# Performance work log

Measured on AMD Instinct MI355X. Metric: run time of the kernel, lower is better.

The kernel has to match this reference:

```python
import jax, jax.numpy as jnp
import numpy as np

N_EMBD = 384
N_HEAD = 6
HEAD_SIZE = N_EMBD // N_HEAD  # 64
B, T, S = 128, 256, 256
EPS = 1e-5


def setup_inputs() -> dict:
    key = jax.random.key(0)
    ks = jax.random.split(key, 20)
    w = lambda k, shape: (jax.random.normal(k, shape, dtype=jnp.float32) * 0.02)
    inp = {
        'x': jax.random.normal(ks[0], (B, T, N_EMBD), dtype=jnp.float32),
        'encoder_output': jax.random.normal(ks[1], (B, S, N_EMBD), dtype=jnp.float32),
        # masked self-attention heads (stacked over heads): [H, C, D]
        'wq1': w(ks[2], (N_HEAD, N_EMBD, HEAD_SIZE)),
        'wk1': w(ks[3], (N_HEAD, N_EMBD, HEAD_SIZE)),
        'wv1': w(ks[4], (N_HEAD, N_EMBD, HEAD_SIZE)),
        'proj1_w': w(ks[5], (N_EMBD, N_EMBD)),
        'proj1_b': jnp.zeros((N_EMBD,), jnp.float32),
        # cross-attention heads
        'wq2': w(ks[6], (N_HEAD, N_EMBD, HEAD_SIZE)),
        'wk2': w(ks[7], (N_HEAD, N_EMBD, HEAD_SIZE)),
        'wv2': w(ks[8], (N_HEAD, N_EMBD, HEAD_SIZE)),
        'proj2_w': w(ks[9], (N_EMBD, N_EMBD)),
        'proj2_b': jnp.zeros((N_EMBD,), jnp.float32),
        # feed-forward
        'ffn_w1': w(ks[10], (N_EMBD, 4 * N_EMBD)),
        'ffn_b1': jnp.zeros((4 * N_EMBD,), jnp.float32),
        'ffn_w2': w(ks[11], (4 * N_EMBD, N_EMBD)),
        'ffn_b2': jnp.zeros((N_EMBD,), jnp.float32),
        # layernorms
        'ln1_g': jnp.ones((N_EMBD,), jnp.float32), 'ln1_b': jnp.zeros((N_EMBD,), jnp.float32),
        'ln2_g': jnp.ones((N_EMBD,), jnp.float32), 'ln2_b': jnp.zeros((N_EMBD,), jnp.float32),
        'ln3_g': jnp.ones((N_EMBD,), jnp.float32), 'ln3_b': jnp.zeros((N_EMBD,), jnp.float32),
    }
    return inp


def _layernorm(x, g, b):
    mu = jnp.mean(x, axis=-1, keepdims=True)
    var = jnp.mean(jnp.square(x - mu), axis=-1, keepdims=True)
    return (x - mu) * jax.lax.rsqrt(var + EPS) * g + b


def _mha(xq, xkv, wq, wk, wv, proj_w, proj_b, causal):
    # NOTE: source scales by C**-0.5 with C = n_embd (not head_size)
    scale = jnp.asarray(N_EMBD, xq.dtype) ** -0.5
    q = jnp.einsum('btc,hcd->bhtd', xq, wq)
    k = jnp.einsum('bsc,hcd->bhsd', xkv, wk)
    v = jnp.einsum('bsc,hcd->bhsd', xkv, wv)
    wei = jnp.einsum('bhtd,bhsd->bhts', q, k) * scale
    if causal:
        Tq, Tk = xq.shape[1], xkv.shape[1]
        mask = jnp.tril(jnp.ones((Tq, Tk), dtype=bool))
        wei = jnp.where(mask, wei, jnp.asarray(-jnp.inf, wei.dtype))
    p = jax.nn.softmax(wei, axis=-1)  # dropout omitted (eval mode)
    o = jnp.einsum('bhts,bhsd->bhtd', p, v)
    Bq, H, Tq, D = o.shape
    o = o.transpose(0, 2, 1, 3).reshape(Bq, Tq, H * D)  # concat heads
    return o @ proj_w + proj_b


def reference(x, encoder_output,
              wq1, wk1, wv1, proj1_w, proj1_b,
              wq2, wk2, wv2, proj2_w, proj2_b,
              ffn_w1, ffn_b1, ffn_w2, ffn_b2,
              ln1_g, ln1_b, ln2_g, ln2_b, ln3_g, ln3_b):
    # x = x + masked self-attn(ln1(x))
    x = x + _mha(_layernorm(x, ln1_g, ln1_b), _layernorm(x, ln1_g, ln1_b),
                 wq1, wk1, wv1, proj1_w, proj1_b, causal=True)
    # x = x + cross-attn(ln2(x), encoder_output)  (no mask)
    x = x + _mha(_layernorm(x, ln2_g, ln2_b), encoder_output,
                 wq2, wk2, wv2, proj2_w, proj2_b, causal=False)
    # x = x + ffwd(ln3(x))
    h = _layernorm(x, ln3_g, ln3_b)
    x = x + (jax.nn.relu(h @ ffn_w1 + ffn_b1) @ ffn_w2 + ffn_b2)
    return x
```

## Files before the change

### kernel.cpp

```cpp
#include <hip/hip_runtime.h>
#include <hip/hip_bf16.h>

#define BB 128
#define TT 256
#define CC 384
#define HH 6
#define DD 64
#define NTOK 32768

typedef __attribute__((ext_vector_type(8))) short short8;
typedef __attribute__((ext_vector_type(4))) float f32x4;

__device__ __forceinline__ unsigned short f2bf(float f) {
  union { float f; unsigned int u; } v; v.f = f;
  unsigned int r = v.u + 0x7fff + ((v.u >> 16) & 1);
  return (unsigned short)(r >> 16);
}

__device__ __forceinline__ void glds16(const void* g, void* l) {
  __builtin_amdgcn_global_load_lds((const __attribute__((address_space(1))) void*)g,
                                   (__attribute__((address_space(3))) void*)l, 16, 0, 0);
}

__device__ __forceinline__ void vm_drain() {
  asm volatile("s_waitcnt vmcnt(0)" ::: "memory");
  __builtin_amdgcn_sched_barrier(0);
}

__global__ __launch_bounds__(256) void pack_all_k(
    const float* __restrict__ wq1, const float* __restrict__ wk1, const float* __restrict__ wv1,
    const float* __restrict__ wq2, const float* __restrict__ wk2, const float* __restrict__ wv2,
    const float* __restrict__ proj1_w, const float* __restrict__ proj2_w,
    const float* __restrict__ ffn_w1, const float* __restrict__ ffn_w2,
    unsigned short* __restrict__ W) {
  int idx = blockIdx.x * 256 + threadIdx.x;
  if (idx < 589824) {
    int sub = idx / 147456, r = idx - sub * 147456;
    const float* src = sub == 0 ? wq1 : sub == 1 ? wk1 : sub == 2 ? wv1 : wq2;
    unsigned short* dst = W + sub * 147456;
    int h = r / 24576, rem = r - h * 24576;
    int c = rem >> 6, d = rem & 63;
    dst[(h * 64 + d) * 384 + c] = f2bf(src[r]);
  } else if (idx < 884736) {
    int t = idx - 589824;
    int sub = t / 147456, r = t - sub * 147456;
    const float* src = sub ? wv2 : wk2;
    unsigned short* dst = W + 589824 + sub * 147456;
    int h = r / 24576, rem = r - h * 24576;
    int c = rem >> 6, d = rem & 63;
    dst[(h * 64 + d) * 384 + c] = f2bf(src[r]);
  } else if (idx < 1179648) {
    int t = idx - 884736;
    int sub = t / 147456, r = t - sub * 147456;
    const float* src = sub ? proj2_w : proj1_w;
    unsigned short* dst = W + 884736 + sub * 147456;
    int c = r / 384, n = r - c * 384;
    dst[n * 384 + c] = f2bf(src[r]);
  } else if (idx < 1769472) {
    int r = idx - 1179648;
    int c = r / 1536, n = r - c * 1536;
    (W + 1179648)[n * 384 + c] = f2bf(ffn_w1[r]);
  } else {
    int r = idx - 1769472;
    int c = r / 384, n = r - c * 384;
    (W + 1769472)[n * 1536 + c] = f2bf(ffn_w2[r]);
  }
}

__global__ __launch_bounds__(256) void ln_k(const float* __restrict__ x,
                                            unsigned short* __restrict__ out,
                                            const float* __restrict__ gamma,
                                            const float* __restrict__ beta) {
  int row = blockIdx.x * 4 + (threadIdx.x >> 6);
  int lane = threadIdx.x & 63;
  const float* xr = x + (size_t)row * CC;
  float v[6];
  float s = 0.f;
#pragma unroll
  for (int j = 0; j < 6; ++j) { v[j] = xr[j * 64 + lane]; s += v[j]; }
#pragma unroll
  for (int m = 1; m < 64; m <<= 1) s += __shfl_xor(s, m);
  float mu = s * (1.0f / CC);
  float vs = 0.f;
#pragma unroll
  for (int j = 0; j < 6; ++j) { float d = v[j] - mu; vs += d * d; }
#pragma unroll
  for (int m = 1; m < 64; m <<= 1) vs += __shfl_xor(vs, m);
  float rs = rsqrtf(vs * (1.0f / CC) + 1e-5f);
  unsigned short* orow = out + (size_t)row * CC;
#pragma unroll
  for (int j = 0; j < 6; ++j) {
    int cidx = j * 64 + lane;
    orow[cidx] = f2bf((v[j] - mu) * rs * gamma[cidx] + beta[cidx]);
  }
}

template <int EPI, bool AF32>
__global__ __launch_bounds__(256) void gemm_k(const void* __restrict__ Ap, int lda,
                                              const unsigned short* __restrict__ Bt, int ldb,
                                              void* __restrict__ Cp, int ldc,
                                              const float* __restrict__ bias,
                                              const float* __restrict__ res, int ldres,
                                              int K, int nx) {
  __shared__ unsigned short smem[16384];
  unsigned short* sA = smem;
  unsigned short* sB = smem + 8192;
  const int tid = threadIdx.x;
  const int chunkg = gridDim.x >> 3;
  const int wg = blockIdx.x;
  const int lg = (wg & 7) * chunkg + (wg >> 3);
  const int bx = lg % nx, by = lg / nx;
  const int m0 = by * 128;
  const int n0 = bx * 128;
  const int wid = tid >> 6, lane = tid & 63;
  const int wr = wid >> 1, wc = wid & 1;
  const int g = lane >> 4, c = lane & 15;

  f32x4 acc[4][4] = {};
  float biasr[4];
  if (EPI >= 1) {
#pragma unroll
    for (int ni = 0; ni < 4; ++ni) biasr[ni] = bias[n0 + wc * 64 + ni * 16 + c];
  }

  for (int k0 = 0; k0 < K; k0 += 64) {
    if constexpr (!AF32) {
#pragma unroll
      for (int t = 0; t < 4; ++t) {
        int chunk = t * 256 + tid;
        int row = chunk >> 3, grp = chunk & 7;
        const unsigned short* Ab = (const unsigned short*)Ap;
        glds16(&Ab[(size_t)(m0 + row) * lda + k0 + ((grp ^ (row & 7)) << 3)], &sA[chunk * 8]);
      }
    } else {
#pragma unroll
      for (int t = 0; t < 4; ++t) {
        int chunk = t * 256 + tid;
        int row = chunk >> 3, grp = chunk & 7;
        int dst = row * 64 + ((grp ^ (row & 7)) << 3);
        const float* Af = (const float*)Ap + (size_t)(m0 + row) * lda + k0 + grp * 8;
        float4 f0 = *(const float4*)Af;
        float4 f1 = *(const float4*)(Af + 4);
        union { unsigned short h[8]; uint4 u; } t2;
        t2.h[0] = f2bf(f0.x); t2.h[1] = f2bf(f0.y); t2.h[2] = f2bf(f0.z); t2.h[3] = f2bf(f0.w);
        t2.h[4] = f2bf(f1.x); t2.h[5] = f2bf(f1.y); t2.h[6] = f2bf(f1.z); t2.h[7] = f2bf(f1.w);
        *(uint4*)&sA[dst] = t2.u;
      }
    }
#pragma unroll
    for (int t = 0; t < 4; ++t) {
      int chunk = t * 256 + tid;
      int row = chunk >> 3, grp = chunk & 7;
      glds16(&Bt[(size_t)(n0 + row) * ldb + k0 + ((grp ^ (row & 7)) << 3)], &sB[chunk * 8]);
    }
    vm_drain();
    __syncthreads();
#pragma unroll
    for (int kk = 0; kk < 2; ++kk) {
      short8 a[4], b[4];
#pragma unroll
      for (int mi = 0; mi < 4; ++mi) {
        int r = wr * 64 + mi * 16 + c;
        a[mi] = *(const short8*)&sA[r * 64 + (((kk * 4 + g) ^ (r & 7)) << 3)];
      }
#pragma unroll
      for (int ni = 0; ni < 4; ++ni) {
        int rb = wc * 64 + ni * 16 + c;
        b[ni] = *(const short8*)&sB[rb * 64 + (((kk * 4 + g) ^ (rb & 7)) << 3)];
      }
#pragma unroll
      for (int mi = 0; mi < 4; ++mi)
#pragma unroll
        for (int ni = 0; ni < 4; ++ni)
          acc[mi][ni] = __builtin_amdgcn_mfma_f32_16x16x32_bf16(a[mi], b[ni], acc[mi][ni], 0, 0, 0);
    }
    __syncthreads();
  }

  if (EPI <= 1) {
#pragma unroll
    for (int mi = 0; mi < 4; ++mi)
#pragma unroll
      for (int ni = 0; ni < 4; ++ni)
#pragma unroll
        for (int i = 0; i < 4; ++i) {
          int row = wr * 64 + mi * 16 + g * 4 + i;
          int col = wc * 64 + ni * 16 + c;
          float v = acc[mi][ni][i];
          if (EPI == 1) v = fmaxf(v + biasr[ni], 0.f);
          int gsw = (col >> 3) ^ ((row >> 2) & 7);
          smem[row * 128 + gsw * 8 + (col & 7)] = f2bf(v);
        }
    __syncthreads();
#pragma unroll
    for (int it = 0; it < 8; ++it) {
      int chunk = it * 256 + tid;
      int row = chunk >> 4, c16 = chunk & 15;
      int gsw = c16 ^ ((row >> 2) & 7);
      *(uint4*)&((unsigned short*)Cp)[(size_t)(m0 + row) * ldc + n0 + c16 * 8] =
          *(const uint4*)&smem[row * 128 + gsw * 8];
    }
  } else {
#pragma unroll
    for (int mi = 0; mi < 4; ++mi)
#pragma unroll
      for (int ni = 0; ni < 4; ++ni)
#pragma unroll
        for (int i = 0; i < 4; ++i) {
          int row = m0 + wr * 64 + mi * 16 + g * 4 + i;
          int col = n0 + wc * 64 + ni * 16 + c;
          float v = acc[mi][ni][i] + biasr[ni] + res[(size_t)row * ldres + col];
          ((float*)Cp)[(size_t)row * ldc + col] = v;
        }
  }
}

__device__ __forceinline__ int vt_off(int d, int sgrp) {
  return d * 256 + ((((sgrp + (d >> 3)) & 31) ^ (d & 7)) << 3);
}

template <bool CAUSAL>
__global__ __launch_bounds__(512, 2) void attn_k(const unsigned short* __restrict__ QKV,
                                                 unsigned short* __restrict__ O) {
  __shared__ unsigned short Ks[256 * 64];
  __shared__ unsigned short Vt[64 * 256];
  __shared__ unsigned short Ps[8][16 * 40];
  const int bh = blockIdx.x >> 1;
  const int half = blockIdx.x & 1;
  const int b = bh / HH, hh = bh - b * HH;
  const int tid = threadIdx.x, wid = tid >> 6, lane = tid & 63;
  const int g = lane >> 4, c = lane & 15;
  const unsigned short* base = QKV + (size_t)b * TT * 1152;

#pragma unroll
  for (int t = 0; t < 4; ++t) {
    int chunk = t * 512 + tid;
    int s = chunk >> 3, grp = chunk & 7;
    *(uint4*)&Ks[s * 64 + ((grp ^ (s & 7)) << 3)] =
        *(const uint4*)&base[(size_t)s * 1152 + 384 + hh * 64 + grp * 8];
    union { unsigned short h[8]; uint4 u; } tv;
    tv.u = *(const uint4*)&base[(size_t)s * 1152 + 768 + hh * 64 + grp * 8];
#pragma unroll
    for (int j = 0; j < 8; ++j) Vt[vt_off(grp * 8 + j, s >> 3) + (s & 7)] = tv.h[j];
  }
  __syncthreads();

  const float scale = 0.05103103630798287f;
  unsigned short* Pw = &Ps[wid][0];
  const int qr0 = half * 128 + wid * 16;

  short8 aq[2];
#pragma unroll
  for (int kk = 0; kk < 2; ++kk)
    aq[kk] = *(const short8*)&QKV[(size_t)(b * TT + qr0 + c) * 1152 + hh * 64 + kk * 32 + g * 8];

  f32x4 sacc[16] = {};
#pragma unroll
  for (int sj = 0; sj < 16; ++sj) {
    if (!CAUSAL || sj * 16 <= qr0) {
      int rk = sj * 16 + c;
      f32x4 z = sacc[sj];
      z = __builtin_amdgcn_mfma_f32_16x16x32_bf16(
          aq[0], *(const short8*)&Ks[rk * 64 + ((g ^ (rk & 7)) << 3)], z, 0, 0, 0);
      z = __builtin_amdgcn_mfma_f32_16x16x32_bf16(
          aq[1], *(const short8*)&Ks[rk * 64 + (((4 + g) ^ (rk & 7)) << 3)], z, 0, 0, 0);
      sacc[sj] = z;
    }
  }

  float inv[4];
#pragma unroll
  for (int i = 0; i < 4; ++i) {
    const int qr = qr0 + g * 4 + i;
    float mx = -1e30f;
#pragma unroll
    for (int sj = 0; sj < 16; ++sj) {
      if (!CAUSAL || sj * 16 <= qr0) {
        int s = sj * 16 + c;
        float v = sacc[sj][i] * scale;
        if (CAUSAL && s > qr) v = -1e30f;
        sacc[sj][i] = v;
        mx = fmaxf(mx, v);
      }
    }
#pragma unroll
    for (int m = 1; m < 16; m <<= 1) mx = fmaxf(mx, __shfl_xor(mx, m));
    float sum = 0.f;
#pragma unroll
    for (int sj = 0; sj < 16; ++sj) {
      if (!CAUSAL || sj * 16 <= qr0) {
        float p = __expf(sacc[sj][i] - mx);
        sacc[sj][i] = p;
        sum += p;
      }
    }
#pragma unroll
    for (int m = 1; m < 16; m <<= 1) sum += __shfl_xor(sum, m);
    inv[i] = 1.0f / sum;
  }

  f32x4 oacc[4] = {};
#pragma unroll
  for (int sk = 0; sk < 8; ++sk) {
    if (!CAUSAL || sk * 32 <= qr0) {
#pragma unroll
      for (int half_sj = 0; half_sj < 2; ++half_sj) {
        int sj = sk * 2 + half_sj;
#pragma unroll
        for (int i = 0; i < 4; ++i)
          Pw[(g * 4 + i) * 40 + half_sj * 16 + c] = f2bf(sacc[sj][i]);
      }
      short8 ap = *(const short8*)&Pw[c * 40 + g * 8];
#pragma unroll
      for (int dj = 0; dj < 4; ++dj) {
        short8 bv = *(const short8*)&Vt[vt_off(dj * 16 + c, sk * 4 + g)];
        oacc[dj] = __builtin_amdgcn_mfma_f32_16x16x32_bf16(ap, bv, oacc[dj], 0, 0, 0);
      }
    }
  }

  __syncthreads();
#pragma unroll
  for (int dj = 0; dj < 4; ++dj)
#pragma unroll
    for (int i = 0; i < 4; ++i) {
      int lr = wid * 16 + g * 4 + i;
      int col = dj * 16 + c;
      int gsw = (col >> 3) ^ ((lr >> 2) & 7);
      Ks[lr * 64 + gsw * 8 + (col & 7)] = f2bf(oacc[dj][i] * inv[i]);
    }
  __syncthreads();
#pragma unroll
  for (int it = 0; it < 2; ++it) {
    int chunk = it * 512 + tid;
    int row = chunk >> 3, c8 = chunk & 7;
    int gsw = c8 ^ ((row >> 2) & 7);
    *(uint4*)&O[(size_t)(b * TT + half * 128 + row) * CC + hh * 64 + c8 * 8] =
        *(const uint4*)&Ks[row * 64 + gsw * 8];
  }
}

extern "C" void kernel_launch(void* const* d_in, const int* in_sizes, int n_in,
                              void* d_out, int out_size, void* d_ws, size_t ws_size,
                              hipStream_t stream) {
  const float* x = (const float*)d_in[0];
  const float* enc = (const float*)d_in[1];
  const float* wq1 = (const float*)d_in[2];
  const float* wk1 = (const float*)d_in[3];
  const float* wv1 = (const float*)d_in[4];
  const float* proj1_w = (const float*)d_in[5];
  const float* proj1_b = (const float*)d_in[6];
  const float* wq2 = (const float*)d_in[7];
  const float* wk2 = (const float*)d_in[8];
  const float* wv2 = (const float*)d_in[9];
  const float* proj2_w = (const float*)d_in[10];
  const float* proj2_b = (const float*)d_in[11];
  const float* ffn_w1 = (const float*)d_in[12];
  const float* ffn_b1 = (const float*)d_in[13];
  const float* ffn_w2 = (const float*)d_in[14];
  const float* ffn_b2 = (const float*)d_in[15];
  const float* ln1_g = (const float*)d_in[16];
  const float* ln1_b = (const float*)d_in[17];
  const float* ln2_g = (const float*)d_in[18];
  const float* ln2_b = (const float*)d_in[19];
  const float* ln3_g = (const float*)d_in[20];
  const float* ln3_b = (const float*)d_in[21];
  float* out = (float*)d_out;

  char* ws = (char*)d_ws;
  const size_t OFF_A = 0;
  const size_t OFF_X = 50331648;
  const size_t OFF_Q = 75497472;
  const size_t OFF_O = 150994944;
  const size_t OFF_W = 176160768;

  float* xc = (float*)(ws + OFF_A);
  unsigned short* xn = (unsigned short*)(ws + OFF_X);
  unsigned short* qkv = (unsigned short*)(ws + OFF_Q);
  unsigned short* h1 = (unsigned short*)(ws + OFF_Q);
  unsigned short* obuf = (unsigned short*)(ws + OFF_O);
  unsigned short* W = (unsigned short*)(ws + OFF_W);

  unsigned short* Wqkv1t = W + 0;
  unsigned short* Wq2t = W + 442368;
  unsigned short* Wkv2t = W + 589824;
  unsigned short* proj1t = W + 884736;
  unsigned short* proj2t = W + 1032192;
  unsigned short* W1t = W + 1179648;
  unsigned short* W2t = W + 1769472;

  pack_all_k<<<9216, 256, 0, stream>>>(wq1, wk1, wv1, wq2, wk2, wv2,
                                       proj1_w, proj2_w, ffn_w1, ffn_w2, W);

  dim3 blk(256);
  ln_k<<<8192, blk, 0, stream>>>(x, xn, ln1_g, ln1_b);
  gemm_k<0, false><<<2304, blk, 0, stream>>>(xn, 384, Wqkv1t, 384, qkv, 1152,
                                             nullptr, nullptr, 0, 384, 9);
  attn_k<true><<<1536, 512, 0, stream>>>(qkv, obuf);
  gemm_k<2, false><<<768, blk, 0, stream>>>(obuf, 384, proj1t, 384, xc, 384,
                                            proj1_b, x, 384, 384, 3);
  ln_k<<<8192, blk, 0, stream>>>(xc, xn, ln2_g, ln2_b);
  gemm_k<0, false><<<768, blk, 0, stream>>>(xn, 384, Wq2t, 384, qkv, 1152,
                                            nullptr, nullptr, 0, 384, 3);
  gemm_k<0, true><<<1536, blk, 0, stream>>>(enc, 384, Wkv2t, 384, qkv + 384, 1152,
                                            nullptr, nullptr, 0, 384, 6);
  attn_k<false><<<1536, 512, 0, stream>>>(qkv, obuf);
  gemm_k<2, false><<<768, blk, 0, stream>>>(obuf, 384, proj2t, 384, xc, 384,
                                            proj2_b, xc, 384, 384, 3);
  ln_k<<<8192, blk, 0, stream>>>(xc, xn, ln3_g, ln3_b);
  gemm_k<1, false><<<3072, blk, 0, stream>>>(xn, 384, W1t, 384, h1, 1536,
                                             ffn_b1, nullptr, 0, 384, 12);
  gemm_k<2, false><<<768, blk, 0, stream>>>(h1, 1536, W2t, 1536, out, 384,
                                            ffn_b2, xc, 384, 1536, 3);
}
```

Before: 415.5 us.

## Use 64-row tiles for residual GEMMs, prefetch residual, tile weight packing

The weight pack kernel now transposes 64x64 tiles through shared memory. Reads are float4 and writes are 16-byte, replacing the scattered per-element transposed stores. The GEMM is templated on the M tile size. The three N=384 residual-epilogue GEMMs use 64-row tiles with twice as many blocks, which should improve occupancy and load balance across CUs. Residual values are also loaded into registers during the last two K iterations, overlapping that load with the MFMA work at the cost of extra registers.

```diff
diff --git a/kernel.cpp b/kernel.cpp
--- a/kernel.cpp
+++ b/kernel.cpp
@@ -27,43 +27,60 @@
   __builtin_amdgcn_sched_barrier(0);
 }
 
-__global__ __launch_bounds__(256) void pack_all_k(
+__global__ __launch_bounds__(256) void pack_t_k(
     const float* __restrict__ wq1, const float* __restrict__ wk1, const float* __restrict__ wv1,
     const float* __restrict__ wq2, const float* __restrict__ wk2, const float* __restrict__ wv2,
     const float* __restrict__ proj1_w, const float* __restrict__ proj2_w,
     const float* __restrict__ ffn_w1, const float* __restrict__ ffn_w2,
     unsigned short* __restrict__ W) {
-  int idx = blockIdx.x * 256 + threadIdx.x;
-  if (idx < 589824) {
-    int sub = idx / 147456, r = idx - sub * 147456;
-    const float* src = sub == 0 ? wq1 : sub == 1 ? wk1 : sub == 2 ? wv1 : wq2;
-    unsigned short* dst = W + sub * 147456;
-    int h = r / 24576, rem = r - h * 24576;
-    int c = rem >> 6, d = rem & 63;
-    dst[(h * 64 + d) * 384 + c] = f2bf(src[r]);
-  } else if (idx < 884736) {
-    int t = idx - 589824;
-    int sub = t / 147456, r = t - sub * 147456;
-    const float* src = sub ? wv2 : wk2;
-    unsigned short* dst = W + 589824 + sub * 147456;
-    int h = r / 24576, rem = r - h * 24576;
-    int c = rem >> 6, d = rem & 63;
-    dst[(h * 64 + d) * 384 + c] = f2bf(src[r]);
-  } else if (idx < 1179648) {
-    int t = idx - 884736;
-    int sub = t / 147456, r = t - sub * 147456;
-    const float* src = sub ? proj2_w : proj1_w;
-    unsigned short* dst = W + 884736 + sub * 147456;
-    int c = r / 384, n = r - c * 384;
-    dst[n * 384 + c] = f2bf(src[r]);
-  } else if (idx < 1769472) {
-    int r = idx - 1179648;
-    int c = r / 1536, n = r - c * 1536;
-    (W + 1179648)[n * 384 + c] = f2bf(ffn_w1[r]);
+  __shared__ unsigned short tile[64 * 72];
+  const int id = blockIdx.x;
+  const int tid = threadIdx.x;
+  const float* src;
+  unsigned short* dst;
+  int ldIn, ldOut, i0, j0;
+  if (id < 216) {
+    int w = id / 36, rem = id - w * 36;
+    int h = rem / 6, tr = rem - h * 6;
+    const float* bases[6] = {wq1, wk1, wv1, wq2, wk2, wv2};
+    const int dstOff[6] = {0, 147456, 294912, 442368, 589824, 737280};
+    src = bases[w] + h * 24576;
+    dst = W + dstOff[w] + h * 24576;
+    ldIn = 64; ldOut = 384; i0 = tr * 64; j0 = 0;
+  } else if (id < 288) {
+    int t = id - 216;
+    int which = t / 36; t -= which * 36;
+    int tr = t / 6, tc = t - tr * 6;
+    src = which ? proj2_w : proj1_w;
+    dst = W + (which ? 1032192 : 884736);
+    ldIn = 384; ldOut = 384; i0 = tr * 64; j0 = tc * 64;
+  } else if (id < 432) {
+    int t = id - 288;
+    int tr = t / 24, tc = t - tr * 24;
+    src = ffn_w1; dst = W + 1179648;
+    ldIn = 1536; ldOut = 384; i0 = tr * 64; j0 = tc * 64;
   } else {
-    int r = idx - 1769472;
-    int c = r / 384, n = r - c * 384;
-    (W + 1769472)[n * 1536 + c] = f2bf(ffn_w2[r]);
+    int t = id - 432;
+    int tr = t / 6, tc = t - tr * 6;
+    src = ffn_w2; dst = W + 1769472;
+    ldIn = 384; ldOut = 1536; i0 = tr * 64; j0 = tc * 64;
+  }
+#pragma unroll
+  for (int p = 0; p < 4; ++p) {
+    int chunk = p * 256 + tid;
+    int r = chunk >> 4, c4 = chunk & 15;
+    float4 f = *(const float4*)&src[(size_t)(i0 + r) * ldIn + j0 + c4 * 4];
+    tile[(c4 * 4 + 0) * 72 + r] = f2bf(f.x);
+    tile[(c4 * 4 + 1) * 72 + r] = f2bf(f.y);
+    tile[(c4 * 4 + 2) * 72 + r] = f2bf(f.z);
+    tile[(c4 * 4 + 3) * 72 + r] = f2bf(f.w);
+  }
+  __syncthreads();
+#pragma unroll
+  for (int p = 0; p < 2; ++p) {
+    int chunk = p * 256 + tid;
+    int j = chunk >> 3, i8 = chunk & 7;
+    *(uint4*)&dst[(size_t)(j0 + j) * ldOut + i0 + i8 * 8] = *(const uint4*)&tile[j * 72 + i8 * 8];
   }
 }
 
@@ -95,47 +112,52 @@
   }
 }
 
-template <int EPI, bool AF32>
+template <int EPI, bool AF32, int BM>
 __global__ __launch_bounds__(256) void gemm_k(const void* __restrict__ Ap, int lda,
                                               const unsigned short* __restrict__ Bt, int ldb,
                                               void* __restrict__ Cp, int ldc,
                                               const float* __restrict__ bias,
                                               const float* __restrict__ res, int ldres,
                                               int K, int nx) {
-  __shared__ unsigned short smem[16384];
+  constexpr int MI = BM / 32;
+  constexpr int APASS = BM * 8 / 256;
+  __shared__ unsigned short smem[BM * 64 + 8192];
   unsigned short* sA = smem;
-  unsigned short* sB = smem + 8192;
+  unsigned short* sB = smem + BM * 64;
   const int tid = threadIdx.x;
   const int chunkg = gridDim.x >> 3;
   const int wg = blockIdx.x;
   const int lg = (wg & 7) * chunkg + (wg >> 3);
   const int bx = lg % nx, by = lg / nx;
-  const int m0 = by * 128;
+  const int m0 = by * BM;
   const int n0 = bx * 128;
   const int wid = tid >> 6, lane = tid & 63;
   const int wr = wid >> 1, wc = wid & 1;
   const int g = lane >> 4, c = lane & 15;
 
-  f32x4 acc[4][4] = {};
+  f32x4 acc[MI][4] = {};
   float biasr[4];
   if (EPI >= 1) {
 #pragma unroll
     for (int ni = 0; ni < 4; ++ni) biasr[ni] = bias[n0 + wc * 64 + ni * 16 + c];
   }
-
-  for (int k0 = 0; k0 < K; k0 += 64) {
+  float resr[MI][4][4];
+
+  const int nt = K >> 6;
+  for (int t = 0; t < nt; ++t) {
+    const int k0 = t * 64;
     if constexpr (!AF32) {
 #pragma unroll
-      for (int t = 0; t < 4; ++t) {
-        int chunk = t * 256 + tid;
+      for (int p = 0; p < APASS; ++p) {
+        int chunk = p * 256 + tid;
         int row = chunk >> 3, grp = chunk & 7;
         const unsigned short* Ab = (const unsigned short*)Ap;
         glds16(&Ab[(size_t)(m0 + row) * lda + k0 + ((grp ^ (row & 7)) << 3)], &sA[chunk * 8]);
       }
     } else {
 #pragma unroll
-      for (int t = 0; t < 4; ++t) {
-        int chunk = t * 256 + tid;
+      for (int p = 0; p < APASS; ++p) {
+        int chunk = p * 256 + tid;
         int row = chunk >> 3, grp = chunk & 7;
         int dst = row * 64 + ((grp ^ (row & 7)) << 3);
         const float* Af = (const float*)Ap + (size_t)(m0 + row) * lda + k0 + grp * 8;
@@ -148,19 +170,31 @@
       }
     }
 #pragma unroll
-    for (int t = 0; t < 4; ++t) {
-      int chunk = t * 256 + tid;
+    for (int p = 0; p < 4; ++p) {
+      int chunk = p * 256 + tid;
       int row = chunk >> 3, grp = chunk & 7;
       glds16(&Bt[(size_t)(n0 + row) * ldb + k0 + ((grp ^ (row & 7)) << 3)], &sB[chunk * 8]);
     }
+    if (EPI == 2 && t >= nt - 2) {
+      int mlo = (t == nt - 2) ? 0 : MI / 2;
+      int mhi = (t == nt - 2) ? MI / 2 : MI;
+      for (int mi = mlo; mi < mhi; ++mi)
+#pragma unroll
+        for (int i = 0; i < 4; ++i) {
+          int row = m0 + wr * (BM / 2) + mi * 16 + g * 4 + i;
+#pragma unroll
+          for (int ni = 0; ni < 4; ++ni)
+            resr[mi][ni][i] = res[(size_t)row * ldres + n0 + wc * 64 + ni * 16 + c];
+        }
+    }
     vm_drain();
     __syncthreads();
 #pragma unroll
     for (int kk = 0; kk < 2; ++kk) {
-      short8 a[4], b[4];
-#pragma unroll
-      for (int mi = 0; mi < 4; ++mi) {
-        int r = wr * 64 + mi * 16 + c;
+      short8 a[MI], b[4];
+#pragma unroll
+      for (int mi = 0; mi < MI; ++mi) {
+        int r = wr * (BM / 2) + mi * 16 + c;
         a[mi] = *(const short8*)&sA[r * 64 + (((kk * 4 + g) ^ (r & 7)) << 3)];
       }
 #pragma unroll
@@ -169,7 +203,7 @@
         b[ni] = *(const short8*)&sB[rb * 64 + (((kk * 4 + g) ^ (rb & 7)) << 3)];
       }
 #pragma unroll
-      for (int mi = 0; mi < 4; ++mi)
+      for (int mi = 0; mi < MI; ++mi)
 #pragma unroll
         for (int ni = 0; ni < 4; ++ni)
           acc[mi][ni] = __builtin_amdgcn_mfma_f32_16x16x32_bf16(a[mi], b[ni], acc[mi][ni], 0, 0, 0);
@@ -179,12 +213,12 @@
 
   if (EPI <= 1) {
 #pragma unroll
-    for (int mi = 0; mi < 4; ++mi)
+    for (int mi = 0; mi < MI; ++mi)
 #pragma unroll
       for (int ni = 0; ni < 4; ++ni)
 #pragma unroll
         for (int i = 0; i < 4; ++i) {
-          int row = wr * 64 + mi * 16 + g * 4 + i;
+          int row = wr * (BM / 2) + mi * 16 + g * 4 + i;
           int col = wc * 64 + ni * 16 + c;
           float v = acc[mi][ni][i];
           if (EPI == 1) v = fmaxf(v + biasr[ni], 0.f);
@@ -193,7 +227,7 @@
         }
     __syncthreads();
 #pragma unroll
-    for (int it = 0; it < 8; ++it) {
+    for (int it = 0; it < BM / 16; ++it) {
       int chunk = it * 256 + tid;
       int row = chunk >> 4, c16 = chunk & 15;
       int gsw = c16 ^ ((row >> 2) & 7);
@@ -202,14 +236,14 @@
     }
   } else {
 #pragma unroll
-    for (int mi = 0; mi < 4; ++mi)
+    for (int mi = 0; mi < MI; ++mi)
 #pragma unroll
       for (int ni = 0; ni < 4; ++ni)
 #pragma unroll
         for (int i = 0; i < 4; ++i) {
-          int row = m0 + wr * 64 + mi * 16 + g * 4 + i;
+          int row = m0 + wr * (BM / 2) + mi * 16 + g * 4 + i;
           int col = n0 + wc * 64 + ni * 16 + c;
-          float v = acc[mi][ni][i] + biasr[ni] + res[(size_t)row * ldres + col];
+          float v = acc[mi][ni][i] + biasr[ni] + resr[mi][ni][i];
           ((float*)Cp)[(size_t)row * ldc + col] = v;
         }
   }
@@ -389,27 +423,27 @@
   unsigned short* W1t = W + 1179648;
   unsigned short* W2t = W + 1769472;
 
-  pack_all_k<<<9216, 256, 0, stream>>>(wq1, wk1, wv1, wq2, wk2, wv2,
-                                       proj1_w, proj2_w, ffn_w1, ffn_w2, W);
+  pack_t_k<<<576, 256, 0, stream>>>(wq1, wk1, wv1, wq2, wk2, wv2,
+                                    proj1_w, proj2_w, ffn_w1, ffn_w2, W);
 
   dim3 blk(256);
   ln_k<<<8192, blk, 0, stream>>>(x, xn, ln1_g, ln1_b);
-  gemm_k<0, false><<<2304, blk, 0, stream>>>(xn, 384, Wqkv1t, 384, qkv, 1152,
-                                             nullptr, nullptr, 0, 384, 9);
+  gemm_k<0, false, 128><<<2304, blk, 0, stream>>>(xn, 384, Wqkv1t, 384, qkv, 1152,
+                                                  nullptr, nullptr, 0, 384, 9);
   attn_k<true><<<1536, 512, 0, stream>>>(qkv, obuf);
-  gemm_k<2, false><<<768, blk, 0, stream>>>(obuf, 384, proj1t, 384, xc, 384,
-                                            proj1_b, x, 384, 384, 3);
+  gemm_k<2, false, 64><<<1536, blk, 0, stream>>>(obuf, 384, proj1t, 384, xc, 384,
+                                                 proj1_b, x, 384, 384, 3);
   ln_k<<<8192, blk, 0, stream>>>(xc, xn, ln2_g, ln2_b);
-  gemm_k<0, false><<<768, blk, 0, stream>>>(xn, 384, Wq2t, 384, qkv, 1152,
-                                            nullptr, nullptr, 0, 384, 3);
-  gemm_k<0, true><<<1536, blk, 0, stream>>>(enc, 384, Wkv2t, 384, qkv + 384, 1152,
-                                            nullptr, nullptr, 0, 384, 6);
+  gemm_k<0, false, 128><<<768, blk, 0, stream>>>(xn, 384, Wq2t, 384, qkv, 1152,
+                                                 nullptr, nullptr, 0, 384, 3);
+  gemm_k<0, true, 128><<<1536, blk, 0, stream>>>(enc, 384, Wkv2t, 384, qkv + 384, 1152,
+                                                 nullptr, nullptr, 0, 384, 6);
   attn_k<false><<<1536, 512, 0, stream>>>(qkv, obuf);
-  gemm_k<2, false><<<768, blk, 0, stream>>>(obuf, 384, proj2t, 384, xc, 384,
-                                            proj2_b, xc, 384, 384, 3);
+  gemm_k<2, false, 64><<<1536, blk, 0, stream>>>(obuf, 384, proj2t, 384, xc, 384,
+                                                 proj2_b, xc, 384, 384, 3);
   ln_k<<<8192, blk, 0, stream>>>(xc, xn, ln3_g, ln3_b);
-  gemm_k<1, false><<<3072, blk, 0, stream>>>(xn, 384, W1t, 384, h1, 1536,
-                                             ffn_b1, nullptr, 0, 384, 12);
-  gemm_k<2, false><<<768, blk, 0, stream>>>(h1, 1536, W2t, 1536, out, 384,
-                                            ffn_b2, xc, 384, 1536, 3);
-}
+  gemm_k<1, false, 128><<<3072, blk, 0, stream>>>(xn, 384, W1t, 384, h1, 1536,
+                                                  ffn_b1, nullptr, 0, 384, 12);
+  gemm_k<2, false, 64><<<1536, blk, 0, stream>>>(h1, 1536, W2t, 1536, out, 384,
+                                                 ffn_b2, xc, 384, 1536, 3);
+}
```

After: 448.4 us. 7.9% more time.
